# Optimization experiments

Hardware: AMD Instinct MI355X
Metric: run time of the kernel (lower is better)

Reference implementation:

```python
import jax, jax.numpy as jnp
import numpy as np

N_NODES = 100000
N_EDGES = 1600000
D_IN = 128
D_OUT = 128


def setup_inputs() -> dict:
    key = jax.random.key(0)
    k1, k2, k3, k4, k5, k6 = jax.random.split(key, 6)
    x = jax.random.normal(k1, (N_NODES, D_IN), dtype=jnp.float32)
    adj_rows = jnp.sort(jax.random.randint(k2, (N_EDGES,), 0, N_NODES, dtype=jnp.int32))
    adj_cols = jax.random.randint(k3, (N_EDGES,), 0, N_NODES, dtype=jnp.int32)
    adj_vals = jax.random.uniform(k4, (N_EDGES,), dtype=jnp.float32)
    weight = jax.random.normal(k5, (D_OUT, D_IN), dtype=jnp.float32) * (1.0 / np.sqrt(D_IN))
    bias = jax.random.normal(k6, (D_OUT,), dtype=jnp.float32) * 0.01
    return {"x": x, "adj_rows": adj_rows, "adj_cols": adj_cols,
            "adj_vals": adj_vals, "weight": weight, "bias": bias}


def reference(x, adj_rows, adj_cols, adj_vals, weight, bias):
    # w_input = inputs @ W.T  -> [N, D_OUT]
    w_input = x @ weight.T
    # SpMM: out[r] = sum_e adj_vals[e] * w_input[cols[e]] for edges with rows[e] == r
    msgs = adj_vals[:, None] * w_input[adj_cols]          # [E, D_OUT]
    agg = jax.ops.segment_sum(msgs, adj_rows, num_segments=N_NODES)
    out = jax.nn.relu(agg + bias)
    return out.astype(jnp.float32)
```

## Files before the change

### kernel.cpp

```cpp
#include <hip/hip_runtime.h>
#include <hip/hip_bf16.h>

#define D 128

typedef __attribute__((ext_vector_type(8))) short bf16x8;
typedef __attribute__((ext_vector_type(4))) float f32x4;

__device__ __forceinline__ unsigned short f2bf(float f) {
    union { float f; unsigned u; } uf{f};
    unsigned r = uf.u + 0x7fffu + ((uf.u >> 16) & 1u);
    return (unsigned short)(r >> 16);
}
__device__ __forceinline__ unsigned pack2(float a, float b) {
    return (unsigned)f2bf(a) | ((unsigned)f2bf(b) << 16);
}
__device__ __forceinline__ float bflo(unsigned u) {
    union { unsigned u; float f; } c{u << 16};
    return c.f;
}
__device__ __forceinline__ float bfhi(unsigned u) {
    union { unsigned u; float f; } c{u & 0xffff0000u};
    return c.f;
}

#define FMA8(A, vv, u) \
    A[0] = fmaf(vv, bflo(u.x), A[0]); A[1] = fmaf(vv, bfhi(u.x), A[1]); \
    A[2] = fmaf(vv, bflo(u.y), A[2]); A[3] = fmaf(vv, bfhi(u.y), A[3]); \
    A[4] = fmaf(vv, bflo(u.z), A[4]); A[5] = fmaf(vv, bfhi(u.z), A[5]); \
    A[6] = fmaf(vv, bflo(u.w), A[6]); A[7] = fmaf(vv, bfhi(u.w), A[7]);

__global__ __launch_bounds__(256) void build_rowptr(const int* __restrict__ rows,
                                                    const float* __restrict__ W,
                                                    unsigned short* __restrict__ wbf,
                                                    int* __restrict__ row_start,
                                                    int* __restrict__ row_end,
                                                    int e) {
    int i = blockIdx.x * 256 + threadIdx.x;
    if (i < D * D) wbf[i] = f2bf(W[i]);
    if (i >= e) return;
    int r = rows[i];
    if (i == 0 || rows[i - 1] != r) row_start[r] = i;
    if (i == e - 1 || rows[i + 1] != r) row_end[r] = i + 1;
}

__global__ __launch_bounds__(256, 3) void gemm_mfma(const float* __restrict__ x,
                                                    const unsigned short* __restrict__ wbf,
                                                    unsigned short* __restrict__ wi,
                                                    int nrows) {
    __shared__ __align__(16) unsigned short Xs[128 * 128];

    const int tid = threadIdx.x;
    const int row0 = blockIdx.x * 128;

#pragma unroll
    for (int it = 0; it < 16; ++it) {
        int f = it * 1024 + tid * 4;
        int r = f >> 7, k = f & 127;
        int idx = (r * 128 + k) ^ ((r & 7) << 3);
        int gr = row0 + r;
        float4 xv = (gr < nrows) ? *(const float4*)(x + (size_t)gr * D + k)
                                 : make_float4(0.f, 0.f, 0.f, 0.f);
        *(uint2*)&Xs[idx] = make_uint2(pack2(xv.x, xv.y), pack2(xv.z, xv.w));
    }
    __syncthreads();

    const int lane = tid & 63;
    const int m_base = (tid >> 6) * 32;
    const int lrow = lane & 15;
    const int lk8 = (lane >> 4) * 8;

    bf16x8 afrag[2][4];
#pragma unroll
    for (int rb = 0; rb < 2; ++rb)
#pragma unroll
        for (int kb = 0; kb < 4; ++kb) {
            int r = m_base + rb * 16 + lrow;
            int k = kb * 32 + lk8;
            int idx = (r * 128 + k) ^ ((r & 7) << 3);
            afrag[rb][kb] = *(const bf16x8*)&Xs[idx];
        }

    f32x4 acc[2][8];
#pragma unroll
    for (int rb = 0; rb < 2; ++rb)
#pragma unroll
        for (int nb = 0; nb < 8; ++nb)
            acc[rb][nb] = (f32x4){0.f, 0.f, 0.f, 0.f};

#pragma unroll
    for (int nb = 0; nb < 8; ++nb) {
#pragma unroll
        for (int kb = 0; kb < 4; ++kb) {
            bf16x8 bfrag = *(const bf16x8*)(wbf + (nb * 16 + lrow) * 128 + kb * 32 + lk8);
            acc[0][nb] = __builtin_amdgcn_mfma_f32_16x16x32_bf16(afrag[0][kb], bfrag, acc[0][nb], 0, 0, 0);
            acc[1][nb] = __builtin_amdgcn_mfma_f32_16x16x32_bf16(afrag[1][kb], bfrag, acc[1][nb], 0, 0, 0);
        }
    }

#pragma unroll
    for (int rb = 0; rb < 2; ++rb)
#pragma unroll
        for (int j = 0; j < 4; ++j) {
            int gr = row0 + m_base + rb * 16 + (lane >> 4) * 4 + j;
            if (gr < nrows) {
#pragma unroll
                for (int nb = 0; nb < 8; ++nb)
                    wi[(size_t)gr * D + nb * 16 + lrow] = f2bf(acc[rb][nb][j]);
            }
        }
}

__global__ __launch_bounds__(256) void spmm_relu(const unsigned short* __restrict__ wi,
                                                 const int* __restrict__ row_start,
                                                 const int* __restrict__ row_end,
                                                 const int* __restrict__ cols,
                                                 const float* __restrict__ vals,
                                                 const float* __restrict__ bias,
                                                 float* __restrict__ out,
                                                 int n) {
    const int lane = threadIdx.x & 63;
    const int r = blockIdx.x * 4 + (threadIdx.x >> 6);
    if (r >= n) return;

    float a0[8] = {0.f, 0.f, 0.f, 0.f, 0.f, 0.f, 0.f, 0.f};
    float a1[8] = {0.f, 0.f, 0.f, 0.f, 0.f, 0.f, 0.f, 0.f};

    const int start = row_start[r];
    if (start >= 0) {
        const int end = row_end[r];
        const int ch = (lane & 15) * 8;
        const int sub = lane >> 4;

        for (int base = start; base < end; base += 64) {
            const int cnt = min(64, end - base);
            int c = 0;
            float v = 0.f;
            if (lane < cnt) {
                c = cols[base + lane];
                v = vals[base + lane];
            }
            for (int q = 0; q * 4 < cnt; q += 4) {
                const int i0 = q * 4 + sub;
                int   c0 = __shfl(c, i0),     c1 = __shfl(c, i0 + 4);
                int   c2 = __shfl(c, i0 + 8), c3 = __shfl(c, i0 + 12);
                float v0 = __shfl(v, i0),     v1 = __shfl(v, i0 + 4);
                float v2 = __shfl(v, i0 + 8), v3 = __shfl(v, i0 + 12);
                uint4 u0 = *(const uint4*)(wi + (size_t)c0 * D + ch);
                uint4 u1 = *(const uint4*)(wi + (size_t)c1 * D + ch);
                uint4 u2 = *(const uint4*)(wi + (size_t)c2 * D + ch);
                uint4 u3 = *(const uint4*)(wi + (size_t)c3 * D + ch);
                FMA8(a0, v0, u0); FMA8(a1, v1, u1);
                FMA8(a0, v2, u2); FMA8(a1, v3, u3);
            }
        }
    }

    float acc[8];
#pragma unroll
    for (int j = 0; j < 8; ++j) {
        float s = a0[j] + a1[j];
        s += __shfl_xor(s, 16);
        s += __shfl_xor(s, 32);
        acc[j] = s;
    }

    if (lane < 16) {
        const int ch = lane * 8;
        float4 b0 = *(const float4*)(bias + ch);
        float4 b1 = *(const float4*)(bias + ch + 4);
        float4 o0, o1;
        o0.x = fmaxf(acc[0] + b0.x, 0.f);
        o0.y = fmaxf(acc[1] + b0.y, 0.f);
        o0.z = fmaxf(acc[2] + b0.z, 0.f);
        o0.w = fmaxf(acc[3] + b0.w, 0.f);
        o1.x = fmaxf(acc[4] + b1.x, 0.f);
        o1.y = fmaxf(acc[5] + b1.y, 0.f);
        o1.z = fmaxf(acc[6] + b1.z, 0.f);
        o1.w = fmaxf(acc[7] + b1.w, 0.f);
        *(float4*)(out + (size_t)r * D + ch) = o0;
        *(float4*)(out + (size_t)r * D + ch + 4) = o1;
    }
}

extern "C" void kernel_launch(void* const* d_in, const int* in_sizes, int n_in,
                              void* d_out, int out_size, void* d_ws, size_t ws_size,
                              hipStream_t stream) {
    const float* x        = (const float*)d_in[0];
    const int*   adj_rows = (const int*)d_in[1];
    const int*   adj_cols = (const int*)d_in[2];
    const float* adj_vals = (const float*)d_in[3];
    const float* weight   = (const float*)d_in[4];
    const float* bias     = (const float*)d_in[5];
    float*       out      = (float*)d_out;

    const int n = in_sizes[0] / D;
    const int e = in_sizes[1];

    unsigned short* wi = (unsigned short*)d_ws;
    size_t off = ((size_t)n * D * sizeof(unsigned short) + 255) & ~(size_t)255;
    int* row_start = (int*)((char*)d_ws + off);
    int* row_end   = row_start + n;
    unsigned short* wbf = (unsigned short*)(row_end + n);

    hipMemsetAsync(row_start, 0xFF, (size_t)n * sizeof(int), stream);
    build_rowptr<<<(e + 255) / 256, 256, 0, stream>>>(adj_rows, weight, wbf,
                                                      row_start, row_end, e);

    gemm_mfma<<<(n + 127) / 128, 256, 0, stream>>>(x, wbf, wi, n);

    spmm_relu<<<(n + 3) / 4, 256, 0, stream>>>(wi, row_start, row_end,
                                               adj_cols, adj_vals, bias, out, n);
}
```

Measured before the change: 104.7 us.

## Pack row pointers, drop memset, direct-load GEMM A, multi-row SpMM waves

```diff
diff --git a/kernel.cpp b/kernel.cpp
--- a/kernel.cpp
+++ b/kernel.cpp
@@ -2,6 +2,7 @@
 #include <hip/hip_bf16.h>
 
 #define D 128
+#define RPW 8
 
 typedef __attribute__((ext_vector_type(8))) short bf16x8;
 typedef __attribute__((ext_vector_type(4))) float f32x4;
@@ -32,40 +33,31 @@
 __global__ __launch_bounds__(256) void build_rowptr(const int* __restrict__ rows,
                                                     const float* __restrict__ W,
                                                     unsigned short* __restrict__ wbf,
-                                                    int* __restrict__ row_start,
-                                                    int* __restrict__ row_end,
-                                                    int e) {
+                                                    int2* __restrict__ rowptr,
+                                                    int e, int n) {
     int i = blockIdx.x * 256 + threadIdx.x;
     if (i < D * D) wbf[i] = f2bf(W[i]);
     if (i >= e) return;
     int r = rows[i];
-    if (i == 0 || rows[i - 1] != r) row_start[r] = i;
-    if (i == e - 1 || rows[i + 1] != r) row_end[r] = i + 1;
-}
-
-__global__ __launch_bounds__(256, 3) void gemm_mfma(const float* __restrict__ x,
-                                                    const unsigned short* __restrict__ wbf,
-                                                    unsigned short* __restrict__ wi,
-                                                    int nrows) {
-    __shared__ __align__(16) unsigned short Xs[128 * 128];
-
-    const int tid = threadIdx.x;
-    const int row0 = blockIdx.x * 128;
-
-#pragma unroll
-    for (int it = 0; it < 16; ++it) {
-        int f = it * 1024 + tid * 4;
-        int r = f >> 7, k = f & 127;
-        int idx = (r * 128 + k) ^ ((r & 7) << 3);
-        int gr = row0 + r;
-        float4 xv = (gr < nrows) ? *(const float4*)(x + (size_t)gr * D + k)
-                                 : make_float4(0.f, 0.f, 0.f, 0.f);
-        *(uint2*)&Xs[idx] = make_uint2(pack2(xv.x, xv.y), pack2(xv.z, xv.w));
-    }
-    __syncthreads();
-
-    const int lane = tid & 63;
-    const int m_base = (tid >> 6) * 32;
+    int prev = (i == 0) ? -1 : rows[i - 1];
+    int next = (i == e - 1) ? n : rows[i + 1];
+    if (prev != r) {
+        rowptr[r].x = i;
+        for (int q = prev + 1; q < r; ++q) rowptr[q] = make_int2(i, i);
+    }
+    if (next != r) {
+        rowptr[r].y = i + 1;
+        if (i == e - 1)
+            for (int q = r + 1; q < n; ++q) rowptr[q] = make_int2(e, e);
+    }
+}
+
+__global__ __launch_bounds__(256) void gemm_mfma(const float* __restrict__ x,
+                                                 const unsigned short* __restrict__ wbf,
+                                                 unsigned short* __restrict__ wi,
+                                                 int nrows) {
+    const int lane = threadIdx.x & 63;
+    const int row0 = blockIdx.x * 128 + (threadIdx.x >> 6) * 32;
     const int lrow = lane & 15;
     const int lk8 = (lane >> 4) * 8;
 
@@ -74,10 +66,15 @@
     for (int rb = 0; rb < 2; ++rb)
 #pragma unroll
         for (int kb = 0; kb < 4; ++kb) {
-            int r = m_base + rb * 16 + lrow;
-            int k = kb * 32 + lk8;
-            int idx = (r * 128 + k) ^ ((r & 7) << 3);
-            afrag[rb][kb] = *(const bf16x8*)&Xs[idx];
+            int gr = min(row0 + rb * 16 + lrow, nrows - 1);
+            const float4* p = (const float4*)(x + (size_t)gr * D + kb * 32 + lk8);
+            float4 f0 = p[0], f1 = p[1];
+            union { bf16x8 v; unsigned u[4]; } cv;
+            cv.u[0] = pack2(f0.x, f0.y);
+            cv.u[1] = pack2(f0.z, f0.w);
+            cv.u[2] = pack2(f1.x, f1.y);
+            cv.u[3] = pack2(f1.z, f1.w);
+            afrag[rb][kb] = cv.v;
         }
 
     f32x4 acc[2][8];
@@ -101,7 +98,7 @@
     for (int rb = 0; rb < 2; ++rb)
 #pragma unroll
         for (int j = 0; j < 4; ++j) {
-            int gr = row0 + m_base + rb * 16 + (lane >> 4) * 4 + j;
+            int gr = row0 + rb * 16 + (lane >> 4) * 4 + j;
             if (gr < nrows) {
 #pragma unroll
                 for (int nb = 0; nb < 8; ++nb)
@@ -111,40 +108,62 @@
 }
 
 __global__ __launch_bounds__(256) void spmm_relu(const unsigned short* __restrict__ wi,
-                                                 const int* __restrict__ row_start,
-                                                 const int* __restrict__ row_end,
+                                                 const int2* __restrict__ rowptr,
                                                  const int* __restrict__ cols,
                                                  const float* __restrict__ vals,
                                                  const float* __restrict__ bias,
                                                  float* __restrict__ out,
                                                  int n) {
     const int lane = threadIdx.x & 63;
-    const int r = blockIdx.x * 4 + (threadIdx.x >> 6);
-    if (r >= n) return;
-
-    float a0[8] = {0.f, 0.f, 0.f, 0.f, 0.f, 0.f, 0.f, 0.f};
-    float a1[8] = {0.f, 0.f, 0.f, 0.f, 0.f, 0.f, 0.f, 0.f};
-
-    const int start = row_start[r];
-    if (start >= 0) {
-        const int end = row_end[r];
-        const int ch = (lane & 15) * 8;
-        const int sub = lane >> 4;
-
-        for (int base = start; base < end; base += 64) {
-            const int cnt = min(64, end - base);
-            int c = 0;
-            float v = 0.f;
-            if (lane < cnt) {
-                c = cols[base + lane];
-                v = vals[base + lane];
-            }
-            for (int q = 0; q * 4 < cnt; q += 4) {
+    const int R0 = (blockIdx.x * 4 + (threadIdx.x >> 6)) * RPW;
+    if (R0 >= n) return;
+    const int nr = min(RPW, n - R0);
+
+    const int2 rp = rowptr[R0 + min(lane, nr - 1)];
+    const int ch = (lane & 15) * 8;
+    const int sub = lane >> 4;
+
+    float4 b0 = *(const float4*)(bias + (lane & 15) * 8);
+    float4 b1 = *(const float4*)(bias + (lane & 15) * 8 + 4);
+
+    int s = __shfl(rp.x, 0), e = __shfl(rp.y, 0);
+    int c = 0; float v = 0.f;
+    { int idx = s + lane; if (idx < e) { c = cols[idx]; v = vals[idx]; } }
+
+    for (int j = 0; j < nr; ++j) {
+        int s_n = 0, e_n = 0, c_n = 0; float v_n = 0.f;
+        if (j + 1 < nr) {
+            s_n = __shfl(rp.x, j + 1); e_n = __shfl(rp.y, j + 1);
+            int idx = s_n + lane; if (idx < e_n) { c_n = cols[idx]; v_n = vals[idx]; }
+        }
+
+        float a0[8] = {0.f, 0.f, 0.f, 0.f, 0.f, 0.f, 0.f, 0.f};
+        float a1[8] = {0.f, 0.f, 0.f, 0.f, 0.f, 0.f, 0.f, 0.f};
+
+        const int cnt = min(e - s, 64);
+        for (int q = 0; q * 4 < cnt; q += 4) {
+            const int i0 = q * 4 + sub;
+            int   c0 = __shfl(c, i0),     c1 = __shfl(c, i0 + 4);
+            int   c2 = __shfl(c, i0 + 8), c3 = __shfl(c, i0 + 12);
+            float v0 = __shfl(v, i0),     v1 = __shfl(v, i0 + 4);
+            float v2 = __shfl(v, i0 + 8), v3 = __shfl(v, i0 + 12);
+            uint4 u0 = *(const uint4*)(wi + (size_t)c0 * D + ch);
+            uint4 u1 = *(const uint4*)(wi + (size_t)c1 * D + ch);
+            uint4 u2 = *(const uint4*)(wi + (size_t)c2 * D + ch);
+            uint4 u3 = *(const uint4*)(wi + (size_t)c3 * D + ch);
+            FMA8(a0, v0, u0); FMA8(a1, v1, u1);
+            FMA8(a0, v2, u2); FMA8(a1, v3, u3);
+        }
+        for (int base = s + 64; base < e; base += 64) {
+            int cc = 0; float vv = 0.f;
+            { int idx = base + lane; if (idx < e) { cc = cols[idx]; vv = vals[idx]; } }
+            const int cnt2 = min(e - base, 64);
+            for (int q = 0; q * 4 < cnt2; q += 4) {
                 const int i0 = q * 4 + sub;
-                int   c0 = __shfl(c, i0),     c1 = __shfl(c, i0 + 4);
-                int   c2 = __shfl(c, i0 + 8), c3 = __shfl(c, i0 + 12);
-                float v0 = __shfl(v, i0),     v1 = __shfl(v, i0 + 4);
-                float v2 = __shfl(v, i0 + 8), v3 = __shfl(v, i0 + 12);
+                int   c0 = __shfl(cc, i0),     c1 = __shfl(cc, i0 + 4);
+                int   c2 = __shfl(cc, i0 + 8), c3 = __shfl(cc, i0 + 12);
+                float v0 = __shfl(vv, i0),     v1 = __shfl(vv, i0 + 4);
+                float v2 = __shfl(vv, i0 + 8), v3 = __shfl(vv, i0 + 12);
                 uint4 u0 = *(const uint4*)(wi + (size_t)c0 * D + ch);
                 uint4 u1 = *(const uint4*)(wi + (size_t)c1 * D + ch);
                 uint4 u2 = *(const uint4*)(wi + (size_t)c2 * D + ch);
@@ -153,32 +172,30 @@
                 FMA8(a0, v2, u2); FMA8(a1, v3, u3);
             }
         }
-    }
-
-    float acc[8];
-#pragma unroll
-    for (int j = 0; j < 8; ++j) {
-        float s = a0[j] + a1[j];
-        s += __shfl_xor(s, 16);
-        s += __shfl_xor(s, 32);
-        acc[j] = s;
-    }
-
-    if (lane < 16) {
-        const int ch = lane * 8;
-        float4 b0 = *(const float4*)(bias + ch);
-        float4 b1 = *(const float4*)(bias + ch + 4);
-        float4 o0, o1;
-        o0.x = fmaxf(acc[0] + b0.x, 0.f);
-        o0.y = fmaxf(acc[1] + b0.y, 0.f);
-        o0.z = fmaxf(acc[2] + b0.z, 0.f);
-        o0.w = fmaxf(acc[3] + b0.w, 0.f);
-        o1.x = fmaxf(acc[4] + b1.x, 0.f);
-        o1.y = fmaxf(acc[5] + b1.y, 0.f);
-        o1.z = fmaxf(acc[6] + b1.z, 0.f);
-        o1.w = fmaxf(acc[7] + b1.w, 0.f);
-        *(float4*)(out + (size_t)r * D + ch) = o0;
-        *(float4*)(out + (size_t)r * D + ch + 4) = o1;
+
+        float r8[8];
+#pragma unroll
+        for (int t = 0; t < 8; ++t) {
+            float sjj = a0[t] + a1[t];
+            sjj += __shfl_xor(sjj, 16);
+            sjj += __shfl_xor(sjj, 32);
+            r8[t] = sjj;
+        }
+        if (lane < 16) {
+            float4 o0, o1;
+            o0.x = fmaxf(r8[0] + b0.x, 0.f);
+            o0.y = fmaxf(r8[1] + b0.y, 0.f);
+            o0.z = fmaxf(r8[2] + b0.z, 0.f);
+            o0.w = fmaxf(r8[3] + b0.w, 0.f);
+            o1.x = fmaxf(r8[4] + b1.x, 0.f);
+            o1.y = fmaxf(r8[5] + b1.y, 0.f);
+            o1.z = fmaxf(r8[6] + b1.z, 0.f);
+            o1.w = fmaxf(r8[7] + b1.w, 0.f);
+            *(float4*)(out + (size_t)(R0 + j) * D + lane * 8) = o0;
+            *(float4*)(out + (size_t)(R0 + j) * D + lane * 8 + 4) = o1;
+        }
+
+        s = s_n; e = e_n; c = c_n; v = v_n;
     }
 }
 
@@ -198,16 +215,15 @@
 
     unsigned short* wi = (unsigned short*)d_ws;
     size_t off = ((size_t)n * D * sizeof(unsigned short) + 255) & ~(size_t)255;
-    int* row_start = (int*)((char*)d_ws + off);
-    int* row_end   = row_start + n;
-    unsigned short* wbf = (unsigned short*)(row_end + n);
-
-    hipMemsetAsync(row_start, 0xFF, (size_t)n * sizeof(int), stream);
+    int2* rowptr = (int2*)((char*)d_ws + off);
+    unsigned short* wbf = (unsigned short*)(rowptr + n);
+
     build_rowptr<<<(e + 255) / 256, 256, 0, stream>>>(adj_rows, weight, wbf,
-                                                      row_start, row_end, e);
+                                                      rowptr, e, n);
 
     gemm_mfma<<<(n + 127) / 128, 256, 0, stream>>>(x, wbf, wi, n);
 
-    spmm_relu<<<(n + 3) / 4, 256, 0, stream>>>(wi, row_start, row_end,
-                                               adj_cols, adj_vals, bias, out, n);
-}
+    const int rows_per_block = 4 * RPW;
+    spmm_relu<<<(n + rows_per_block - 1) / rows_per_block, 256, 0, stream>>>(
+        wi, rowptr, adj_cols, adj_vals, bias, out, n);
+}
```

Measured after the change: 100.9 us. -3.6%, faster.
